# Kernel optimization log

Hardware: AMD Instinct MI355X
Metric: run time of the kernel (lower is better)

Reference implementation:

```python
import jax, jax.numpy as jnp
import numpy as np

H = 8  # num_heads (init kwarg)

def setup_inputs() -> dict:
    key = jax.random.key(0)
    k1, k2, k3, k4 = jax.random.split(key, 4)
    B, S, E = 4, 2048, 512
    x = jax.random.normal(k1, (B, S, E), dtype=jnp.float32)
    # 'normal' keras initializer ~ N(0, 0.05)
    Wq = jax.random.normal(k2, (E, E), dtype=jnp.float32) * 0.05
    Wk = jax.random.normal(k3, (E, E), dtype=jnp.float32) * 0.05
    Wv = jax.random.normal(k4, (E, E), dtype=jnp.float32) * 0.05
    return {"x": x, "Wq": Wq, "Wk": Wk, "Wv": Wv}

def _split_heads(t):
    # [B,S,E] -> [H,B,S,E/H]; matches tf.stack(tf.split(t, H, axis=2))
    B, S, E = t.shape
    return t.reshape(B, S, H, E // H).transpose(2, 0, 1, 3)

def reference(x, Wq, Wk, Wv):
    B, S, E = x.shape
    q = _split_heads(jnp.einsum('bse,ef->bsf', x, Wq))  # [H,B,S,dh]
    k = _split_heads(jnp.einsum('bse,ef->bsf', x, Wk))
    v = _split_heads(jnp.einsum('bse,ef->bsf', x, Wv))
    # NOTE: original has NO 1/sqrt(d) scaling
    scores = jnp.einsum('hbqd,hbkd->hbqk', q, k)         # [H,B,S,S]
    attn = jax.nn.softmax(scores, axis=-1)
    effect = jnp.einsum('hbqk,hbkd->hbqd', attn, v)      # [H,B,S,dh]
    # tf.concat(tf.split(effect, H), axis=-1) + squeeze == merge heads on last dim
    out = effect.transpose(1, 2, 0, 3).reshape(B, S, E)  # [B,S,E]
    return (out, x)
```

## Files before the change

kernel.cpp:

```cpp
#include <hip/hip_runtime.h>

typedef _Float16 f16x8 __attribute__((ext_vector_type(8)));
typedef __fp16 h16x2 __attribute__((ext_vector_type(2)));
typedef float f32x4 __attribute__((ext_vector_type(4)));
typedef float f32x16 __attribute__((ext_vector_type(16)));

#define GF(r) ((((r)&3)) ^ (((r)>>2)&3))
#define LOG2E 1.44269504088896f

#define GLD16(gp, lp) __builtin_amdgcn_global_load_lds( \
    (const __attribute__((address_space(1))) void*)(gp), \
    (__attribute__((address_space(3))) void*)(lp), 16, 0, 0)

__global__ void cvt_x_kernel(const float4* __restrict__ x4, f16x8* __restrict__ xh,
                             float4* __restrict__ xc, int n8) {
    int i = blockIdx.x * 256 + threadIdx.x;
    if (i >= n8) return;
    float4 a = x4[2 * i], b = x4[2 * i + 1];
    xc[2 * i] = a;
    xc[2 * i + 1] = b;
    f16x8 h;
    h[0] = (_Float16)a.x; h[1] = (_Float16)a.y; h[2] = (_Float16)a.z; h[3] = (_Float16)a.w;
    h[4] = (_Float16)b.x; h[5] = (_Float16)b.y; h[6] = (_Float16)b.z; h[7] = (_Float16)b.w;
    xh[i] = h;
}

__global__ void cvt_w_kernel(const float* __restrict__ Wq, const float* __restrict__ Wk,
                             const float* __restrict__ Wv, _Float16* __restrict__ wt) {
    int j = blockIdx.x * 256 + threadIdx.x;
    if (j >= 786432) return;
    int mat = j >> 18;
    int r = (j >> 9) & 511;
    int n = j & 511;
    const float* W = (mat == 0) ? Wq : ((mat == 1) ? Wk : Wv);
    float v = W[r * 512 + n];
    wt[(size_t)mat * 262144 + (size_t)n * 512 + r] = (_Float16)v;
}

__global__ __launch_bounds__(256, 2) void gemm_qkv(
    const _Float16* __restrict__ xh, const _Float16* __restrict__ wt,
    _Float16* __restrict__ qh, _Float16* __restrict__ kh, _Float16* __restrict__ vt) {
    __shared__ __align__(16) char gsm[49152];
    const int mat = blockIdx.y;
    const _Float16* wp = wt + (size_t)mat * 262144;
    const int mtile = blockIdx.x >> 2, ntile = blockIdx.x & 3;
    const int tid = threadIdx.x, lane = tid & 63;
    const int g = lane >> 4, c = lane & 15;
    const int wid = tid >> 6, wm = wid >> 1, wn = wid & 1;

    f32x4 acc[4][4];
#pragma unroll
    for (int i = 0; i < 4; ++i)
#pragma unroll
        for (int j = 0; j < 4; ++j) acc[i][j] = (f32x4){0.f, 0.f, 0.f, 0.f};

    const int row0 = tid >> 2, p0 = tid & 3;

    auto GSTAGE = [&](int buf, int ks) {
        _Float16* la_ = (_Float16*)(gsm + buf * 16384);
        _Float16* lb_ = (_Float16*)(gsm + buf * 16384 + 8192);
        int r = row0, pp = p0 ^ GF(r);
        GLD16(xh + (size_t)(mtile * 128 + r) * 512 + ks * 32 + pp * 8, &la_[tid * 8]);
        GLD16(wp + (size_t)(ntile * 128 + r) * 512 + ks * 32 + pp * 8, &lb_[tid * 8]);
        r = 64 + row0; pp = p0 ^ GF(r);
        GLD16(xh + (size_t)(mtile * 128 + r) * 512 + ks * 32 + pp * 8, &la_[(256 + tid) * 8]);
        GLD16(wp + (size_t)(ntile * 128 + r) * 512 + ks * 32 + pp * 8, &lb_[(256 + tid) * 8]);
    };

    auto GTILE = [&](int ks) {
        const _Float16* la = (const _Float16*)(gsm + (ks % 3) * 16384);
        const _Float16* lb = (const _Float16*)(gsm + (ks % 3) * 16384 + 8192);
        f16x8 af[4], bf[4];
#pragma unroll
        for (int i = 0; i < 4; ++i) {
            int ra = wm * 64 + i * 16 + c;
            af[i] = *(const f16x8*)&la[ra * 32 + ((g ^ GF(ra)) * 8)];
            int rb = wn * 64 + i * 16 + c;
            bf[i] = *(const f16x8*)&lb[rb * 32 + ((g ^ GF(rb)) * 8)];
        }
        __builtin_amdgcn_s_setprio(1);
#pragma unroll
        for (int mi = 0; mi < 4; ++mi)
#pragma unroll
            for (int ni = 0; ni < 4; ++ni)
                acc[mi][ni] = __builtin_amdgcn_mfma_f32_16x16x32_f16(af[mi], bf[ni], acc[mi][ni], 0, 0, 0);
        __builtin_amdgcn_s_setprio(0);
    };

    GSTAGE(0, 0); GSTAGE(1, 1);
#pragma unroll 1
    for (int ks = 0; ks < 14; ++ks) {
        asm volatile("s_waitcnt vmcnt(4)" ::: "memory");
        __builtin_amdgcn_s_barrier();
        __builtin_amdgcn_sched_barrier(0);
        GSTAGE((ks + 2) % 3, ks + 2);
        GTILE(ks);
    }
    asm volatile("s_waitcnt vmcnt(4)" ::: "memory");
    __builtin_amdgcn_s_barrier();
    GTILE(14);
    asm volatile("s_waitcnt vmcnt(0)" ::: "memory");
    __builtin_amdgcn_s_barrier();
    GTILE(15);

#pragma unroll
    for (int mi = 0; mi < 4; ++mi)
#pragma unroll
        for (int ni = 0; ni < 4; ++ni)
#pragma unroll
            for (int r = 0; r < 4; ++r) {
                int m = mtile * 128 + wm * 64 + mi * 16 + g * 4 + r;
                int n = ntile * 128 + wn * 64 + ni * 16 + c;
                _Float16 hv = (_Float16)acc[mi][ni][r];
                if (mat == 0) {
                    qh[(size_t)m * 512 + n] = hv;
                } else if (mat == 1) {
                    kh[(size_t)m * 512 + n] = hv;
                } else {
                    int h = n >> 6, d = n & 63, bb = m >> 11, s = m & 2047;
                    vt[(((size_t)h * 4 + bb) * 64 + d) * 2048 + s] = hv;
                }
            }
}

__global__ __launch_bounds__(512, 4) void attn_kernel(
    const _Float16* __restrict__ qh, const _Float16* __restrict__ kh,
    const _Float16* __restrict__ vt, float* __restrict__ out) {
    __shared__ __align__(16) char smem[65536];

    const int bid = blockIdx.x;
    const int xcd = bid & 7, idx = bid >> 3;
    const int hb = xcd * 4 + (idx >> 4);
    const int qblk = idx & 15;
    const int h = hb >> 2, b = hb & 3;
    const int tid = threadIdx.x, lane = tid & 63, wid = tid >> 6;
    const int qg = wid & 3, half = wid >> 2;
    const int q = lane & 31, hi = lane >> 5;

    const int qrow0 = qblk * 128 + qg * 32;
    const _Float16* qp = qh + ((size_t)b * 2048 + qrow0) * 512 + h * 64;
    const _Float16* kp = kh + (size_t)b * 2048 * 512 + h * 64;
    const _Float16* vp = vt + (size_t)hb * 64 * 2048;

    const int srow = tid >> 3;
    const int ssw = (tid & 7) ^ (srow & 7);

    auto STAGE = [&](int i) {
        char* base = smem + (i & 1) * 32768;
        GLD16(kp + ((size_t)(i * 64 + srow) * 512) + ssw * 8, (_Float16*)(base) + tid * 8);
        GLD16(vp + (size_t)srow * 2048 + i * 64 + ssw * 8, (_Float16*)(base + 8192) + tid * 8);
        GLD16(kp + ((size_t)((16 + i) * 64 + srow) * 512) + ssw * 8, (_Float16*)(base + 16384) + tid * 8);
        GLD16(vp + (size_t)srow * 2048 + (16 + i) * 64 + ssw * 8, (_Float16*)(base + 24576) + tid * 8);
    };

    f16x8 aQ[4];
#pragma unroll
    for (int kc = 0; kc < 4; ++kc)
        aQ[kc] = *(const f16x8*)(qp + (size_t)q * 512 + kc * 16 + hi * 8);

    float mrow = -1e30f, lrow = 0.f;
    f32x16 o0, o1;
#pragma unroll
    for (int i = 0; i < 16; ++i) { o0[i] = 0.f; o1[i] = 0.f; }

    const h16x2 ONE2 = {(__fp16)1.0f, (__fp16)1.0f};

    auto TILE = [&](int it) {
        const _Float16* kb = (const _Float16*)(smem + (it & 1) * 32768 + half * 16384);
        const _Float16* vb = kb + 4096;

        f32x16 s0, s1;
        __builtin_amdgcn_s_setprio(1);
        {
            f32x16 z0, z1;
#pragma unroll
            for (int i = 0; i < 16; ++i) { z0[i] = 0.f; z1[i] = 0.f; }
            const int r0 = q, r1 = 32 + q, sw = q & 7;
#pragma unroll
            for (int kc = 0; kc < 4; ++kc) {
                f16x8 ak0 = *(const f16x8*)&kb[r0 * 64 + (((2 * kc + hi) ^ sw) * 8)];
                f16x8 ak1 = *(const f16x8*)&kb[r1 * 64 + (((2 * kc + hi) ^ sw) * 8)];
                z0 = __builtin_amdgcn_mfma_f32_32x32x16_f16(ak0, aQ[kc], z0, 0, 0, 0);
                z1 = __builtin_amdgcn_mfma_f32_32x32x16_f16(ak1, aQ[kc], z1, 0, 0, 0);
            }
            s0 = z0; s1 = z1;
        }
        __builtin_amdgcn_s_setprio(0);

        float pm;
        {
            float m0 = fmaxf(fmaxf(fmaxf(s0[0], s0[1]), s0[2]), s0[3]);
            float m1 = fmaxf(fmaxf(fmaxf(s0[4], s0[5]), s0[6]), s0[7]);
            float m2 = fmaxf(fmaxf(fmaxf(s0[8], s0[9]), s0[10]), s0[11]);
            float m3 = fmaxf(fmaxf(fmaxf(s0[12], s0[13]), s0[14]), s0[15]);
            float m4 = fmaxf(fmaxf(fmaxf(s1[0], s1[1]), s1[2]), s1[3]);
            float m5 = fmaxf(fmaxf(fmaxf(s1[4], s1[5]), s1[6]), s1[7]);
            float m6 = fmaxf(fmaxf(fmaxf(s1[8], s1[9]), s1[10]), s1[11]);
            float m7 = fmaxf(fmaxf(fmaxf(s1[12], s1[13]), s1[14]), s1[15]);
            float t0 = fmaxf(fmaxf(m0, m1), m2);
            float t1 = fmaxf(fmaxf(m3, m4), m5);
            float t2 = fmaxf(m6, m7);
            pm = fmaxf(fmaxf(t0, t1), t2);
        }
        pm = fmaxf(pm, __shfl_xor(pm, 32));
        if (__any(pm > mrow + 8.0f)) {
            const float nm = fmaxf(mrow, pm);
            const float e = __builtin_amdgcn_exp2f((mrow - nm) * LOG2E);
            mrow = nm;
            lrow *= e;
            o0 *= e;
            o1 *= e;
        }
        const float nm2 = mrow * LOG2E;

#pragma unroll
        for (int i = 0; i < 16; ++i)
            s0[i] = __builtin_amdgcn_exp2f(fmaf(s0[i], LOG2E, -nm2));
#pragma unroll
        for (int i = 0; i < 16; ++i)
            s1[i] = __builtin_amdgcn_exp2f(fmaf(s1[i], LOG2E, -nm2));

        f16x8 pf[4];
        float rs = 0.f;
#pragma unroll
        for (int kb2 = 0; kb2 < 2; ++kb2) {
            const f32x16& sv = kb2 ? s1 : s0;
            h16x2 p0 = __builtin_amdgcn_cvt_pkrtz(sv[0], sv[1]);
            h16x2 p1 = __builtin_amdgcn_cvt_pkrtz(sv[2], sv[3]);
            h16x2 p2 = __builtin_amdgcn_cvt_pkrtz(sv[4], sv[5]);
            h16x2 p3 = __builtin_amdgcn_cvt_pkrtz(sv[6], sv[7]);
            h16x2 p4 = __builtin_amdgcn_cvt_pkrtz(sv[8], sv[9]);
            h16x2 p5 = __builtin_amdgcn_cvt_pkrtz(sv[10], sv[11]);
            h16x2 p6 = __builtin_amdgcn_cvt_pkrtz(sv[12], sv[13]);
            h16x2 p7 = __builtin_amdgcn_cvt_pkrtz(sv[14], sv[15]);
            rs = __builtin_amdgcn_fdot2(p0, ONE2, rs, false);
            rs = __builtin_amdgcn_fdot2(p1, ONE2, rs, false);
            rs = __builtin_amdgcn_fdot2(p2, ONE2, rs, false);
            rs = __builtin_amdgcn_fdot2(p3, ONE2, rs, false);
            rs = __builtin_amdgcn_fdot2(p4, ONE2, rs, false);
            rs = __builtin_amdgcn_fdot2(p5, ONE2, rs, false);
            rs = __builtin_amdgcn_fdot2(p6, ONE2, rs, false);
            rs = __builtin_amdgcn_fdot2(p7, ONE2, rs, false);
            unsigned t0 = __builtin_bit_cast(unsigned, p0);
            unsigned t1 = __builtin_bit_cast(unsigned, p1);
            unsigned t2 = __builtin_bit_cast(unsigned, p2);
            unsigned t3 = __builtin_bit_cast(unsigned, p3);
            unsigned t4 = __builtin_bit_cast(unsigned, p4);
            unsigned t5 = __builtin_bit_cast(unsigned, p5);
            unsigned t6 = __builtin_bit_cast(unsigned, p6);
            unsigned t7 = __builtin_bit_cast(unsigned, p7);
            asm volatile("v_permlane32_swap_b32 %0, %1" : "+v"(t0), "+v"(t2));
            asm volatile("v_permlane32_swap_b32 %0, %1" : "+v"(t1), "+v"(t3));
            asm volatile("v_permlane32_swap_b32 %0, %1" : "+v"(t4), "+v"(t6));
            asm volatile("v_permlane32_swap_b32 %0, %1" : "+v"(t5), "+v"(t7));
            uint4 u0; u0.x = t0; u0.y = t1; u0.z = t2; u0.w = t3;
            uint4 u1; u1.x = t4; u1.y = t5; u1.z = t6; u1.w = t7;
            pf[2 * kb2 + 0] = __builtin_bit_cast(f16x8, u0);
            pf[2 * kb2 + 1] = __builtin_bit_cast(f16x8, u1);
        }
        lrow += rs;

        __builtin_amdgcn_s_setprio(1);
        {
            const int d0 = q, d1 = 32 + q, sw = q & 7;
#pragma unroll
            for (int ck = 0; ck < 4; ++ck) {
                f16x8 av0 = *(const f16x8*)&vb[d0 * 64 + (((2 * ck + hi) ^ sw) * 8)];
                f16x8 av1 = *(const f16x8*)&vb[d1 * 64 + (((2 * ck + hi) ^ sw) * 8)];
                o0 = __builtin_amdgcn_mfma_f32_32x32x16_f16(av0, pf[ck], o0, 0, 0, 0);
                o1 = __builtin_amdgcn_mfma_f32_32x32x16_f16(av1, pf[ck], o1, 0, 0, 0);
            }
        }
        __builtin_amdgcn_s_setprio(0);
    };

    STAGE(0);
#pragma unroll 1
    for (int it = 0; it < 16; ++it) {
        asm volatile("s_waitcnt vmcnt(0)" ::: "memory");
        __builtin_amdgcn_s_barrier();
        __builtin_amdgcn_sched_barrier(0);
        if (it < 15) STAGE(it + 1);
        TILE(it);
    }

    lrow += __shfl_xor(lrow, 32);
    __builtin_amdgcn_s_barrier();

    float* xg = (float*)smem + qg * 2112;
    if (half) {
#pragma unroll
        for (int i = 0; i < 16; ++i) {
            xg[i * 64 + lane] = o0[i];
            xg[(16 + i) * 64 + lane] = o1[i];
        }
        if (!hi) { xg[2048 + q] = mrow; xg[2080 + q] = lrow; }
    }
    __syncthreads();
    if (!half) {
        const float m_b = xg[2048 + q], l_b = xg[2080 + q];
        const float m = fmaxf(mrow, m_b);
        const float e_a = __builtin_amdgcn_exp2f((mrow - m) * LOG2E);
        const float e_b = __builtin_amdgcn_exp2f((m_b - m) * LOG2E);
        const float inv = 1.0f / (lrow * e_a + l_b * e_b);
        const float sa = e_a * inv, sb = e_b * inv;
#pragma unroll
        for (int i = 0; i < 16; ++i) {
            o0[i] = o0[i] * sa + xg[i * 64 + lane] * sb;
            o1[i] = o1[i] * sa + xg[(16 + i) * 64 + lane] * sb;
        }
        asm volatile("s_waitcnt lgkmcnt(0)" ::: "memory");
#pragma unroll
        for (int i = 0; i < 16; ++i) {
            int dr = (i & 3) + 8 * (i >> 2) + 4 * hi;
            xg[dr * 33 + q] = o0[i];
            xg[(32 + dr) * 33 + q] = o1[i];
        }
        __builtin_amdgcn_s_waitcnt(0);
        const int d0c = (lane & 15) * 4;
#pragma unroll
        for (int i2 = 0; i2 < 8; ++i2) {
            int qr = 4 * i2 + (lane >> 4);
            float4 v;
            v.x = xg[(d0c + 0) * 33 + qr];
            v.y = xg[(d0c + 1) * 33 + qr];
            v.z = xg[(d0c + 2) * 33 + qr];
            v.w = xg[(d0c + 3) * 33 + qr];
            *(float4*)(out + ((size_t)b * 2048 + qrow0 + qr) * 512 + h * 64 + d0c) = v;
        }
    }
}

extern "C" void kernel_launch(void* const* d_in, const int* in_sizes, int n_in,
                              void* d_out, int out_size, void* d_ws, size_t ws_size,
                              hipStream_t stream) {
    const float* x = (const float*)d_in[0];
    const float* Wq = (const float*)d_in[1];
    const float* Wk = (const float*)d_in[2];
    const float* Wv = (const float*)d_in[3];
    float* out = (float*)d_out;
    float* xcopy = out + 4194304;

    char* ws = (char*)d_ws;
    _Float16* xh = (_Float16*)ws;
    _Float16* wt = (_Float16*)(ws + (size_t)(10u << 20));
    _Float16* qh = (_Float16*)(ws + (size_t)(12u << 20));
    _Float16* kh = (_Float16*)(ws + (size_t)(20u << 20));
    _Float16* vt = (_Float16*)(ws + (size_t)(28u << 20));

    cvt_x_kernel<<<2048, 256, 0, stream>>>((const float4*)x, (f16x8*)xh, (float4*)xcopy, 524288);
    cvt_w_kernel<<<3072, 256, 0, stream>>>(Wq, Wk, Wv, wt);
    gemm_qkv<<<dim3(256, 3), 256, 0, stream>>>(xh, wt, qh, kh, vt);
    attn_kernel<<<512, 512, 0, stream>>>(qh, kh, vt, out);
}
```

Before: 93.54 us.

## Halve attention KV tile to 32 keys and merge conversion kernels into one launch

The attention kernel now stages 32-key K/V tiles per half instead of 64. That halves LDS from 64KB to 36KB and trims the s1/pf registers, and launch bounds rise to 8 blocks per CU to allow higher occupancy. The loop doubles to 32 iterations, so there are more barriers and softmax rescale checks per key, and the LDS swizzle patterns are redefined. The two x and W conversion kernels are also fused into a single launch to save launch overhead.

```diff
diff --git a/kernel.cpp b/kernel.cpp
--- a/kernel.cpp
+++ b/kernel.cpp
@@ -12,29 +12,29 @@
     (const __attribute__((address_space(1))) void*)(gp), \
     (__attribute__((address_space(3))) void*)(lp), 16, 0, 0)
 
-__global__ void cvt_x_kernel(const float4* __restrict__ x4, f16x8* __restrict__ xh,
-                             float4* __restrict__ xc, int n8) {
-    int i = blockIdx.x * 256 + threadIdx.x;
-    if (i >= n8) return;
-    float4 a = x4[2 * i], b = x4[2 * i + 1];
-    xc[2 * i] = a;
-    xc[2 * i + 1] = b;
-    f16x8 h;
-    h[0] = (_Float16)a.x; h[1] = (_Float16)a.y; h[2] = (_Float16)a.z; h[3] = (_Float16)a.w;
-    h[4] = (_Float16)b.x; h[5] = (_Float16)b.y; h[6] = (_Float16)b.z; h[7] = (_Float16)b.w;
-    xh[i] = h;
-}
-
-__global__ void cvt_w_kernel(const float* __restrict__ Wq, const float* __restrict__ Wk,
-                             const float* __restrict__ Wv, _Float16* __restrict__ wt) {
-    int j = blockIdx.x * 256 + threadIdx.x;
-    if (j >= 786432) return;
-    int mat = j >> 18;
-    int r = (j >> 9) & 511;
-    int n = j & 511;
-    const float* W = (mat == 0) ? Wq : ((mat == 1) ? Wk : Wv);
-    float v = W[r * 512 + n];
-    wt[(size_t)mat * 262144 + (size_t)n * 512 + r] = (_Float16)v;
+__global__ void cvt_all_kernel(const float4* __restrict__ x4, f16x8* __restrict__ xh,
+                               float4* __restrict__ xc,
+                               const float* __restrict__ Wq, const float* __restrict__ Wk,
+                               const float* __restrict__ Wv, _Float16* __restrict__ wt) {
+    const int blk = blockIdx.x;
+    if (blk < 2048) {
+        int i = blk * 256 + threadIdx.x;
+        float4 a = x4[2 * i], b = x4[2 * i + 1];
+        xc[2 * i] = a;
+        xc[2 * i + 1] = b;
+        f16x8 h;
+        h[0] = (_Float16)a.x; h[1] = (_Float16)a.y; h[2] = (_Float16)a.z; h[3] = (_Float16)a.w;
+        h[4] = (_Float16)b.x; h[5] = (_Float16)b.y; h[6] = (_Float16)b.z; h[7] = (_Float16)b.w;
+        xh[i] = h;
+    } else {
+        int j = (blk - 2048) * 256 + threadIdx.x;
+        int mat = j >> 18;
+        int r = (j >> 9) & 511;
+        int n = j & 511;
+        const float* W = (mat == 0) ? Wq : ((mat == 1) ? Wk : Wv);
+        float v = W[r * 512 + n];
+        wt[(size_t)mat * 262144 + (size_t)n * 512 + r] = (_Float16)v;
+    }
 }
 
 __global__ __launch_bounds__(256, 2) void gemm_qkv(
@@ -123,10 +123,10 @@
             }
 }
 
-__global__ __launch_bounds__(512, 4) void attn_kernel(
+__global__ __launch_bounds__(512, 8) void attn_kernel(
     const _Float16* __restrict__ qh, const _Float16* __restrict__ kh,
     const _Float16* __restrict__ vt, float* __restrict__ out) {
-    __shared__ __align__(16) char smem[65536];
+    __shared__ __align__(16) char smem[36864];
 
     const int bid = blockIdx.x;
     const int xcd = bid & 7, idx = bid >> 3;
@@ -142,15 +142,17 @@
     const _Float16* kp = kh + (size_t)b * 2048 * 512 + h * 64;
     const _Float16* vp = vt + (size_t)hb * 64 * 2048;
 
-    const int srow = tid >> 3;
-    const int ssw = (tid & 7) ^ (srow & 7);
+    const int sHalf = tid >> 8, stt = tid & 255;
+    const int krow = stt >> 3;
+    const int kch = (stt & 7) ^ ((krow ^ (krow >> 3)) & 7);
+    const int vrow = stt >> 2;
+    const int vch = (stt & 3) ^ ((vrow ^ (vrow >> 2)) & 3);
 
     auto STAGE = [&](int i) {
-        char* base = smem + (i & 1) * 32768;
-        GLD16(kp + ((size_t)(i * 64 + srow) * 512) + ssw * 8, (_Float16*)(base) + tid * 8);
-        GLD16(vp + (size_t)srow * 2048 + i * 64 + ssw * 8, (_Float16*)(base + 8192) + tid * 8);
-        GLD16(kp + ((size_t)((16 + i) * 64 + srow) * 512) + ssw * 8, (_Float16*)(base + 16384) + tid * 8);
-        GLD16(vp + (size_t)srow * 2048 + (16 + i) * 64 + ssw * 8, (_Float16*)(base + 24576) + tid * 8);
+        char* base = smem + (i & 1) * 16384;
+        const int kvt = sHalf * 32 + i;
+        GLD16(kp + ((size_t)(kvt * 32 + krow) * 512) + kch * 8, (_Float16*)base + tid * 8);
+        GLD16(vp + (size_t)vrow * 2048 + kvt * 32 + vch * 8, (_Float16*)(base + 8192) + tid * 8);
     };
 
     f16x8 aQ[4];
@@ -164,26 +166,26 @@
     for (int i = 0; i < 16; ++i) { o0[i] = 0.f; o1[i] = 0.f; }
 
     const h16x2 ONE2 = {(__fp16)1.0f, (__fp16)1.0f};
+    const int swk = (q ^ (q >> 3)) & 7;
+    const int swv0 = (q ^ (q >> 2)) & 3;
+    const int swv1 = ((32 + q) ^ ((32 + q) >> 2)) & 3;
 
     auto TILE = [&](int it) {
-        const _Float16* kb = (const _Float16*)(smem + (it & 1) * 32768 + half * 16384);
-        const _Float16* vb = kb + 4096;
-
-        f32x16 s0, s1;
+        const _Float16* kb = (const _Float16*)(smem + (it & 1) * 16384 + half * 4096);
+        const _Float16* vb = (const _Float16*)(smem + (it & 1) * 16384 + 8192 + half * 4096);
+
+        f32x16 s0;
         __builtin_amdgcn_s_setprio(1);
         {
-            f32x16 z0, z1;
-#pragma unroll
-            for (int i = 0; i < 16; ++i) { z0[i] = 0.f; z1[i] = 0.f; }
-            const int r0 = q, r1 = 32 + q, sw = q & 7;
+            f32x16 z;
+#pragma unroll
+            for (int i = 0; i < 16; ++i) z[i] = 0.f;
 #pragma unroll
             for (int kc = 0; kc < 4; ++kc) {
-                f16x8 ak0 = *(const f16x8*)&kb[r0 * 64 + (((2 * kc + hi) ^ sw) * 8)];
-                f16x8 ak1 = *(const f16x8*)&kb[r1 * 64 + (((2 * kc + hi) ^ sw) * 8)];
-                z0 = __builtin_amdgcn_mfma_f32_32x32x16_f16(ak0, aQ[kc], z0, 0, 0, 0);
-                z1 = __builtin_amdgcn_mfma_f32_32x32x16_f16(ak1, aQ[kc], z1, 0, 0, 0);
+                f16x8 ak = *(const f16x8*)&kb[q * 64 + (((2 * kc + hi) ^ swk) * 8)];
+                z = __builtin_amdgcn_mfma_f32_32x32x16_f16(ak, aQ[kc], z, 0, 0, 0);
             }
-            s0 = z0; s1 = z1;
+            s0 = z;
         }
         __builtin_amdgcn_s_setprio(0);
 
@@ -193,14 +195,7 @@
             float m1 = fmaxf(fmaxf(fmaxf(s0[4], s0[5]), s0[6]), s0[7]);
             float m2 = fmaxf(fmaxf(fmaxf(s0[8], s0[9]), s0[10]), s0[11]);
             float m3 = fmaxf(fmaxf(fmaxf(s0[12], s0[13]), s0[14]), s0[15]);
-            float m4 = fmaxf(fmaxf(fmaxf(s1[0], s1[1]), s1[2]), s1[3]);
-            float m5 = fmaxf(fmaxf(fmaxf(s1[4], s1[5]), s1[6]), s1[7]);
-            float m6 = fmaxf(fmaxf(fmaxf(s1[8], s1[9]), s1[10]), s1[11]);
-            float m7 = fmaxf(fmaxf(fmaxf(s1[12], s1[13]), s1[14]), s1[15]);
-            float t0 = fmaxf(fmaxf(m0, m1), m2);
-            float t1 = fmaxf(fmaxf(m3, m4), m5);
-            float t2 = fmaxf(m6, m7);
-            pm = fmaxf(fmaxf(t0, t1), t2);
+            pm = fmaxf(fmaxf(m0, m1), fmaxf(m2, m3));
         }
         pm = fmaxf(pm, __shfl_xor(pm, 32));
         if (__any(pm > mrow + 8.0f)) {
@@ -216,23 +211,18 @@
 #pragma unroll
         for (int i = 0; i < 16; ++i)
             s0[i] = __builtin_amdgcn_exp2f(fmaf(s0[i], LOG2E, -nm2));
-#pragma unroll
-        for (int i = 0; i < 16; ++i)
-            s1[i] = __builtin_amdgcn_exp2f(fmaf(s1[i], LOG2E, -nm2));
-
-        f16x8 pf[4];
+
+        f16x8 pf[2];
         float rs = 0.f;
-#pragma unroll
-        for (int kb2 = 0; kb2 < 2; ++kb2) {
-            const f32x16& sv = kb2 ? s1 : s0;
-            h16x2 p0 = __builtin_amdgcn_cvt_pkrtz(sv[0], sv[1]);
-            h16x2 p1 = __builtin_amdgcn_cvt_pkrtz(sv[2], sv[3]);
-            h16x2 p2 = __builtin_amdgcn_cvt_pkrtz(sv[4], sv[5]);
-            h16x2 p3 = __builtin_amdgcn_cvt_pkrtz(sv[6], sv[7]);
-            h16x2 p4 = __builtin_amdgcn_cvt_pkrtz(sv[8], sv[9]);
-            h16x2 p5 = __builtin_amdgcn_cvt_pkrtz(sv[10], sv[11]);
-            h16x2 p6 = __builtin_amdgcn_cvt_pkrtz(sv[12], sv[13]);
-            h16x2 p7 = __builtin_amdgcn_cvt_pkrtz(sv[14], sv[15]);
+        {
+            h16x2 p0 = __builtin_amdgcn_cvt_pkrtz(s0[0], s0[1]);
+            h16x2 p1 = __builtin_amdgcn_cvt_pkrtz(s0[2], s0[3]);
+            h16x2 p2 = __builtin_amdgcn_cvt_pkrtz(s0[4], s0[5]);
+            h16x2 p3 = __builtin_amdgcn_cvt_pkrtz(s0[6], s0[7]);
+            h16x2 p4 = __builtin_amdgcn_cvt_pkrtz(s0[8], s0[9]);
+            h16x2 p5 = __builtin_amdgcn_cvt_pkrtz(s0[10], s0[11]);
+            h16x2 p6 = __builtin_amdgcn_cvt_pkrtz(s0[12], s0[13]);
+            h16x2 p7 = __builtin_amdgcn_cvt_pkrtz(s0[14], s0[15]);
             rs = __builtin_amdgcn_fdot2(p0, ONE2, rs, false);
             rs = __builtin_amdgcn_fdot2(p1, ONE2, rs, false);
             rs = __builtin_amdgcn_fdot2(p2, ONE2, rs, false);
@@ -255,18 +245,17 @@
             asm volatile("v_permlane32_swap_b32 %0, %1" : "+v"(t5), "+v"(t7));
             uint4 u0; u0.x = t0; u0.y = t1; u0.z = t2; u0.w = t3;
             uint4 u1; u1.x = t4; u1.y = t5; u1.z = t6; u1.w = t7;
-            pf[2 * kb2 + 0] = __builtin_bit_cast(f16x8, u0);
-            pf[2 * kb2 + 1] = __builtin_bit_cast(f16x8, u1);
+            pf[0] = __builtin_bit_cast(f16x8, u0);
+            pf[1] = __builtin_bit_cast(f16x8, u1);
         }
         lrow += rs;
 
         __builtin_amdgcn_s_setprio(1);
         {
-            const int d0 = q, d1 = 32 + q, sw = q & 7;
-#pragma unroll
-            for (int ck = 0; ck < 4; ++ck) {
-                f16x8 av0 = *(const f16x8*)&vb[d0 * 64 + (((2 * ck + hi) ^ sw) * 8)];
-                f16x8 av1 = *(const f16x8*)&vb[d1 * 64 + (((2 * ck + hi) ^ sw) * 8)];
+#pragma unroll
+            for (int ck = 0; ck < 2; ++ck) {
+                f16x8 av0 = *(const f16x8*)&vb[q * 32 + (((2 * ck + hi) ^ swv0) * 8)];
+                f16x8 av1 = *(const f16x8*)&vb[(32 + q) * 32 + (((2 * ck + hi) ^ swv1) * 8)];
                 o0 = __builtin_amdgcn_mfma_f32_32x32x16_f16(av0, pf[ck], o0, 0, 0, 0);
                 o1 = __builtin_amdgcn_mfma_f32_32x32x16_f16(av1, pf[ck], o1, 0, 0, 0);
             }
@@ -276,11 +265,11 @@
 
     STAGE(0);
 #pragma unroll 1
-    for (int it = 0; it < 16; ++it) {
+    for (int it = 0; it < 32; ++it) {
         asm volatile("s_waitcnt vmcnt(0)" ::: "memory");
         __builtin_amdgcn_s_barrier();
         __builtin_amdgcn_sched_barrier(0);
-        if (it < 15) STAGE(it + 1);
+        if (it < 31) STAGE(it + 1);
         TILE(it);
     }
 
@@ -348,8 +337,8 @@
     _Float16* kh = (_Float16*)(ws + (size_t)(20u << 20));
     _Float16* vt = (_Float16*)(ws + (size_t)(28u << 20));
 
-    cvt_x_kernel<<<2048, 256, 0, stream>>>((const float4*)x, (f16x8*)xh, (float4*)xcopy, 524288);
-    cvt_w_kernel<<<3072, 256, 0, stream>>>(Wq, Wk, Wv, wt);
+    cvt_all_kernel<<<5120, 256, 0, stream>>>((const float4*)x, (f16x8*)xh, (float4*)xcopy,
+                                             Wq, Wk, Wv, wt);
     gemm_qkv<<<dim3(256, 3), 256, 0, stream>>>(xh, wt, qh, kh, vt);
     attn_kernel<<<512, 512, 0, stream>>>(qh, kh, vt, out);
 }
```

Result: slower. 181.7 us (+94.3%).
